# Performance work log

Measured on AMD Instinct MI355X. Metric: run time of the kernel, lower is better.

## Reference

```python
import jax, jax.numpy as jnp
import numpy as np

B, C, H, W = 8, 256, 32, 32
E = 256       # embedding_dim
K = 8192      # n_embed
COMMIT = 1.0


def setup_inputs() -> dict:
    key = jax.random.key(0)
    k1, k2, k3, k4 = jax.random.split(key, 4)
    z = jax.random.normal(k1, (B, C, H, W), dtype=jnp.float32)
    proj_w = jax.random.normal(k2, (E, C), dtype=jnp.float32) * (1.0 / np.sqrt(C))
    proj_b = jax.random.normal(k3, (E,), dtype=jnp.float32) * 0.01
    # torch init: uniform(-1/n_embed, 1/n_embed)
    embed = jax.random.uniform(k4, (K, E), dtype=jnp.float32, minval=-1.0 / K, maxval=1.0 / K)
    return {"z": z, "proj_w": proj_w, "proj_b": proj_b, "embed": embed}


def reference(z, proj_w, proj_b, embed):
    # 1x1 conv == per-pixel linear; output in NHWC layout (matches permute(0,2,3,1))
    z_e = jnp.einsum('bchw,ec->bhwe', z, proj_w) + proj_b            # [B,H,W,E]
    flat = z_e.reshape(-1, E)                                        # [BHW,E]
    # squared euclidean distance to each codebook entry
    dist = (jnp.sum(flat * flat, axis=1, keepdims=True)
            - 2.0 * flat @ embed.T
            + jnp.sum(embed * embed, axis=1)[None, :])               # [BHW,K]
    embed_ind = jnp.argmin(dist, axis=1).reshape(B, H, W)            # int indices
    z_q = embed[embed_ind]                                           # gather -> [B,H,W,E]
    sg = jax.lax.stop_gradient
    diff = (COMMIT * jnp.mean((sg(z_q) - z_e) ** 2)
            + jnp.mean((z_q - sg(z_e)) ** 2))
    z_q_st = z_e + sg(z_q - z_e)  # straight-through estimator
    return (z_q_st, diff, embed_ind)
```

## Files before the change

### kernel.cpp

```cpp
#include <hip/hip_runtime.h>

#define OUT_ZQ   0
#define OUT_DIFF 2097152
#define OUT_IND  2097153

#define WS_AMIN   0
#define WS_A      65536
#define WS_N      98304
#define WS_EMAX   131072
#define WS_DLIST  131136
#define WS_DCNT   196672
#define WS_PART   196688
#define WS_CCNT   200784
#define WS_CND    200848
#define WS_BQ     594064
#define WS_B3V    1118352
#define WS_ZH3    1310720
#define WS_ZL3    5505024
#define WS_EH3    9699328
#define WS_EL3    13893632
#define WS_BIG_END 18087936ULL
#define CAND_CAP  98304

typedef unsigned long long u64t;
typedef __attribute__((ext_vector_type(8))) short bf16x8;
typedef __attribute__((ext_vector_type(4))) float f32x4;

__device__ inline unsigned short bf16rn(float f) {
    unsigned u = __float_as_uint(f);
    return (unsigned short)((u + 0x7fffu + ((u >> 16) & 1u)) >> 16);
}
__device__ inline float bf16tof(unsigned short h) { return __uint_as_float(((unsigned)h) << 16); }
__device__ inline float valf(u64t k) { return __uint_as_float((unsigned)(k >> 32)); }

#define INITKEY ((((u64t)0x7F7FFFFFu) << 32) | 0xFFFFu)

__global__ __launch_bounds__(256) void k_init(u64t* __restrict__ amin,
                                              int* __restrict__ dcnt,
                                              unsigned* __restrict__ e2) {
    const int i = blockIdx.x * 256 + threadIdx.x;
    amin[i] = ~0ULL;
    if (i < 4) dcnt[i] = 0;
    if (i == 4) *e2 = 0u;
}

__global__ __launch_bounds__(256) void k_ze_np(const float* __restrict__ z,
                                               const float* __restrict__ pw,
                                               const float* __restrict__ pb,
                                               float* __restrict__ ze) {
    __shared__ float lz[32][16];
    const int t   = threadIdx.x;
    const int b   = blockIdx.x >> 6;
    const int hw0 = (blockIdx.x & 63) * 16;

    float acc[16];
#pragma unroll
    for (int p = 0; p < 16; ++p) acc[p] = 0.0f;

    for (int cc = 0; cc < 256; cc += 32) {
        float4 wv[8];
        const float4* wsrc = reinterpret_cast<const float4*>(pw + (size_t)t * 256 + cc);
#pragma unroll
        for (int i = 0; i < 8; ++i) wv[i] = wsrc[i];
        float zv[2];
#pragma unroll
        for (int i = 0; i < 2; ++i) {
            const int f = t + i * 256;
            zv[i] = z[(size_t)(b * 256 + cc + (f >> 4)) * 1024 + hw0 + (f & 15)];
        }
        __syncthreads();
#pragma unroll
        for (int i = 0; i < 2; ++i) {
            const int f = t + i * 256;
            lz[f >> 4][f & 15] = zv[i];
        }
        __syncthreads();
#define ZSTEP(CL, WL) {                                                     \
    const float4 q0 = *reinterpret_cast<const float4*>(&lz[CL][0]);         \
    const float4 q1 = *reinterpret_cast<const float4*>(&lz[CL][4]);         \
    const float4 q2 = *reinterpret_cast<const float4*>(&lz[CL][8]);         \
    const float4 q3 = *reinterpret_cast<const float4*>(&lz[CL][12]);        \
    acc[0]  = __fadd_rn(acc[0],  __fmul_rn(q0.x, WL));                      \
    acc[1]  = __fadd_rn(acc[1],  __fmul_rn(q0.y, WL));                      \
    acc[2]  = __fadd_rn(acc[2],  __fmul_rn(q0.z, WL));                      \
    acc[3]  = __fadd_rn(acc[3],  __fmul_rn(q0.w, WL));                      \
    acc[4]  = __fadd_rn(acc[4],  __fmul_rn(q1.x, WL));                      \
    acc[5]  = __fadd_rn(acc[5],  __fmul_rn(q1.y, WL));                      \
    acc[6]  = __fadd_rn(acc[6],  __fmul_rn(q1.z, WL));                      \
    acc[7]  = __fadd_rn(acc[7],  __fmul_rn(q1.w, WL));                      \
    acc[8]  = __fadd_rn(acc[8],  __fmul_rn(q2.x, WL));                      \
    acc[9]  = __fadd_rn(acc[9],  __fmul_rn(q2.y, WL));                      \
    acc[10] = __fadd_rn(acc[10], __fmul_rn(q2.z, WL));                      \
    acc[11] = __fadd_rn(acc[11], __fmul_rn(q2.w, WL));                      \
    acc[12] = __fadd_rn(acc[12], __fmul_rn(q3.x, WL));                      \
    acc[13] = __fadd_rn(acc[13], __fmul_rn(q3.y, WL));                      \
    acc[14] = __fadd_rn(acc[14], __fmul_rn(q3.z, WL));                      \
    acc[15] = __fadd_rn(acc[15], __fmul_rn(q3.w, WL)); }
#pragma unroll
        for (int c8 = 0; c8 < 8; ++c8) {
            const float4 wq = wv[c8];
            ZSTEP(c8 * 4 + 0, wq.x)
            ZSTEP(c8 * 4 + 1, wq.y)
            ZSTEP(c8 * 4 + 2, wq.z)
            ZSTEP(c8 * 4 + 3, wq.w)
        }
#undef ZSTEP
    }
    const float bb = pb[t];
#pragma unroll
    for (int p = 0; p < 16; ++p)
        ze[(size_t)(b * 1024 + hw0 + p) * 256 + t] = __fadd_rn(acc[p], bb);
}

__global__ __launch_bounds__(256) void k_rowstats(const float* __restrict__ ze,
                                                  const float* __restrict__ embed,
                                                  float* __restrict__ A,
                                                  float* __restrict__ Nf,
                                                  unsigned* __restrict__ e2) {
    const int gid = blockIdx.x * 256 + threadIdx.x;
    const float* row = (gid < 8192) ? (ze + (size_t)gid * 256)
                                    : (embed + (size_t)(gid - 8192) * 256);
    float blk[2];
#pragma unroll
    for (int half = 0; half < 2; ++half) {
        const float4* r4 = reinterpret_cast<const float4*>(row + half * 128);
        float r[8];
#pragma unroll
        for (int i = 0; i < 16; ++i) {
            const float4 a = r4[i * 2], b = r4[i * 2 + 1];
            const float s[8] = {__fmul_rn(a.x, a.x), __fmul_rn(a.y, a.y),
                                __fmul_rn(a.z, a.z), __fmul_rn(a.w, a.w),
                                __fmul_rn(b.x, b.x), __fmul_rn(b.y, b.y),
                                __fmul_rn(b.z, b.z), __fmul_rn(b.w, b.w)};
            if (i == 0) {
#pragma unroll
                for (int j = 0; j < 8; ++j) r[j] = s[j];
            } else {
#pragma unroll
                for (int j = 0; j < 8; ++j) r[j] = __fadd_rn(r[j], s[j]);
            }
        }
        blk[half] = __fadd_rn(__fadd_rn(__fadd_rn(r[0], r[1]), __fadd_rn(r[2], r[3])),
                              __fadd_rn(__fadd_rn(r[4], r[5]), __fadd_rn(r[6], r[7])));
    }
    const float res = __fadd_rn(blk[0], blk[1]);
    if (gid < 8192) A[gid] = res;
    else {
        Nf[gid - 8192] = res;
        float mx = res;
        for (int off = 32; off; off >>= 1) mx = fmaxf(mx, __shfl_down(mx, off, 64));
        if ((threadIdx.x & 63) == 0) atomicMax(e2, __float_as_uint(mx));
    }
}

__global__ __launch_bounds__(256) void k_cvt(const float* __restrict__ ze,
                                             const float* __restrict__ embed,
                                             unsigned short* __restrict__ zh3,
                                             unsigned short* __restrict__ zl3,
                                             unsigned short* __restrict__ eh3,
                                             unsigned short* __restrict__ el3,
                                             int* __restrict__ ccnt) {
    const int gid = blockIdx.x * 256 + threadIdx.x;
    if (gid == 0) *ccnt = 0;
    const int row = gid >> 5;
    const int c0  = (gid & 31) * 8;
    const bool isz = (row < 8192);
    const float* src = (isz ? ze + (size_t)row * 256 : embed + (size_t)(row - 8192) * 256) + c0;
    const float4 v0 = reinterpret_cast<const float4*>(src)[0];
    const float4 v1 = reinterpret_cast<const float4*>(src)[1];
    float x[8] = {v0.x, v0.y, v0.z, v0.w, v1.x, v1.y, v1.z, v1.w};
    if (isz) {
#pragma unroll
        for (int i = 0; i < 8; ++i) x[i] = __fmul_rn(2.0f, x[i]);
    }
    unsigned short hv[8], lv[8];
#pragma unroll
    for (int i = 0; i < 8; ++i) {
        hv[i] = bf16rn(x[i]);
        lv[i] = bf16rn(__fsub_rn(x[i], bf16tof(hv[i])));
    }
    const int ci = c0 >> 5, lg = (c0 >> 3) & 3;
    if (isz) {
        const int pt = row >> 6, ti = (row >> 4) & 3, lr = row & 15;
        const int lane = lg * 16 + lr;
        const size_t off = ((size_t)(ci * 128 + pt) * 4 + ti) * 512 + (size_t)lane * 8;
        *reinterpret_cast<ushort4*>(zh3 + off)     = make_ushort4(hv[0], hv[1], hv[2], hv[3]);
        *reinterpret_cast<ushort4*>(zh3 + off + 4) = make_ushort4(hv[4], hv[5], hv[6], hv[7]);
        *reinterpret_cast<ushort4*>(zl3 + off)     = make_ushort4(lv[0], lv[1], lv[2], lv[3]);
        *reinterpret_cast<ushort4*>(zl3 + off + 4) = make_ushort4(lv[4], lv[5], lv[6], lv[7]);
    } else {
        const int k = row - 8192;
        const int ks = k >> 11, ksub = (k >> 8) & 7, w = (k >> 6) & 3, tj = (k >> 4) & 3, lr = k & 15;
        const int lane = lg * 16 + lr;
        const size_t off = (((size_t)((ks * 8 + ksub) * 8 + ci) * 16) + w * 4 + tj) * 512 + (size_t)lane * 8;
        *reinterpret_cast<ushort4*>(eh3 + off)     = make_ushort4(hv[0], hv[1], hv[2], hv[3]);
        *reinterpret_cast<ushort4*>(eh3 + off + 4) = make_ushort4(hv[4], hv[5], hv[6], hv[7]);
        *reinterpret_cast<ushort4*>(el3 + off)     = make_ushort4(lv[0], lv[1], lv[2], lv[3]);
        *reinterpret_cast<ushort4*>(el3 + off + 4) = make_ushort4(lv[4], lv[5], lv[6], lv[7]);
    }
}

__global__ __launch_bounds__(256, 2) void k_mfma(const float* __restrict__ A,
                                                 const float* __restrict__ Nf,
                                                 const unsigned short* __restrict__ zh3,
                                                 const unsigned short* __restrict__ zl3,
                                                 const unsigned short* __restrict__ eh3,
                                                 const unsigned short* __restrict__ el3,
                                                 u64t* __restrict__ bq12,
                                                 float* __restrict__ b3v) {
    __shared__ u64t  mrgk[64][4][2];
    __shared__ float mrgv[64][4];
    const int t = threadIdx.x;
    const int ks = blockIdx.x & 3, pt = blockIdx.x >> 2;
    const int pix0 = pt * 64;
    const int w = t >> 6, l = t & 63;
    const int lg = l >> 4, lr = l & 15;

    float a_reg[4][4];
#pragma unroll
    for (int ti = 0; ti < 4; ++ti)
#pragma unroll
        for (int r = 0; r < 4; ++r)
            a_reg[ti][r] = A[pix0 + ti * 16 + lg * 4 + r];

    u64t b1[4][4], b2[4][4];
    float bv[4][4];
#pragma unroll
    for (int ti = 0; ti < 4; ++ti)
#pragma unroll
        for (int r = 0; r < 4; ++r) { b1[ti][r] = INITKEY; b2[ti][r] = INITKEY; bv[ti][r] = 3.402823466e+38f; }

    const size_t zoff0 = (size_t)pt * 2048 + (size_t)l * 8;
    for (int ksub = 0; ksub < 8; ++ksub) {
        f32x4 acc[4][4];
#pragma unroll
        for (int ti = 0; ti < 4; ++ti)
#pragma unroll
            for (int tj = 0; tj < 4; ++tj) acc[ti][tj] = (f32x4)(0.0f);

        const size_t ebase = (size_t)(ks * 8 + ksub) * 65536 + (size_t)w * 2048 + (size_t)l * 8;
#pragma unroll 2
        for (int ci = 0; ci < 8; ++ci) {
            const size_t zo = zoff0 + (size_t)ci * 262144;
            const size_t eo = ebase + (size_t)ci * 8192;
            bf16x8 az[4], alz[4], be[4], ble[4];
#pragma unroll
            for (int ti = 0; ti < 4; ++ti) {
                az[ti]  = *reinterpret_cast<const bf16x8*>(zh3 + zo + (size_t)ti * 512);
                alz[ti] = *reinterpret_cast<const bf16x8*>(zl3 + zo + (size_t)ti * 512);
            }
#pragma unroll
            for (int tj = 0; tj < 4; ++tj) {
                be[tj]  = *reinterpret_cast<const bf16x8*>(eh3 + eo + (size_t)tj * 512);
                ble[tj] = *reinterpret_cast<const bf16x8*>(el3 + eo + (size_t)tj * 512);
            }
#pragma unroll
            for (int tj = 0; tj < 4; ++tj)
#pragma unroll
                for (int ti = 0; ti < 4; ++ti) {
                    acc[ti][tj] = __builtin_amdgcn_mfma_f32_16x16x32_bf16(az[ti],  be[tj],  acc[ti][tj], 0, 0, 0);
                    acc[ti][tj] = __builtin_amdgcn_mfma_f32_16x16x32_bf16(az[ti],  ble[tj], acc[ti][tj], 0, 0, 0);
                    acc[ti][tj] = __builtin_amdgcn_mfma_f32_16x16x32_bf16(alz[ti], be[tj],  acc[ti][tj], 0, 0, 0);
                }
        }
#pragma unroll
        for (int tj = 0; tj < 4; ++tj) {
            const int kk = ks * 2048 + ksub * 256 + w * 64 + tj * 16 + lr;
            const float nk = Nf[kk];
#pragma unroll
            for (int ti = 0; ti < 4; ++ti)
#pragma unroll
                for (int r = 0; r < 4; ++r) {
                    const float vv = __fadd_rn(__fsub_rn(a_reg[ti][r], acc[ti][tj][r]), nk);
                    const u64t key = ((u64t)__float_as_uint(vv) << 32) | (unsigned)kk;
                    if (key < b2[ti][r]) {
                        bv[ti][r] = valf(b2[ti][r]);
                        if (key < b1[ti][r]) { b2[ti][r] = b1[ti][r]; b1[ti][r] = key; }
                        else                 { b2[ti][r] = key; }
                    } else {
                        bv[ti][r] = fminf(bv[ti][r], vv);
                    }
                }
        }
    }
#pragma unroll
    for (int ti = 0; ti < 4; ++ti)
#pragma unroll
        for (int r = 0; r < 4; ++r) {
            u64t k1 = b1[ti][r], k2 = b2[ti][r];
            float v3 = bv[ti][r];
#pragma unroll
            for (int m = 1; m <= 8; m <<= 1) {
                const u64t o1 = __shfl_xor(k1, m, 64);
                const u64t o2 = __shfl_xor(k2, m, 64);
                const float ov = __shfl_xor(v3, m, 64);
                const u64t n1 = (k1 < o1) ? k1 : o1;
                const u64t X  = (k1 < o1) ? o1 : k1;
                const u64t Y  = (k2 < o2) ? k2 : o2;
                const u64t n2 = (X < Y) ? X : Y;
                const u64t t4 = (X < Y) ? Y : X;
                v3 = fminf(fminf(v3, ov), valf(t4));
                k1 = n1; k2 = n2;
            }
            b1[ti][r] = k1; b2[ti][r] = k2; bv[ti][r] = v3;
        }
    if (lr == 0) {
#pragma unroll
        for (int ti = 0; ti < 4; ++ti)
#pragma unroll
            for (int r = 0; r < 4; ++r) {
                const int pxl = ti * 16 + lg * 4 + r;
                mrgk[pxl][w][0] = b1[ti][r];
                mrgk[pxl][w][1] = b2[ti][r];
                mrgv[pxl][w]    = bv[ti][r];
            }
    }
    __syncthreads();
    if (t < 64) {
        u64t K1 = INITKEY, K2 = INITKEY;
        float V3 = 3.402823466e+38f;
#pragma unroll
        for (int w4 = 0; w4 < 4; ++w4) {
            const u64t o1 = mrgk[t][w4][0], o2 = mrgk[t][w4][1];
            const float ov = mrgv[t][w4];
            const u64t n1 = (K1 < o1) ? K1 : o1;
            const u64t X  = (K1 < o1) ? o1 : K1;
            const u64t Y  = (K2 < o2) ? K2 : o2;
            const u64t n2 = (X < Y) ? X : Y;
            const u64t t4 = (X < Y) ? Y : X;
            V3 = fminf(fminf(V3, ov), valf(t4));
            K1 = n1; K2 = n2;
        }
        bq12[((size_t)(ks * 2 + 0)) * 8192 + pix0 + t] = K1;
        bq12[((size_t)(ks * 2 + 1)) * 8192 + pix0 + t] = K2;
        b3v[(size_t)ks * 8192 + pix0 + t] = V3;
    }
}

__global__ __launch_bounds__(256) void k_sel(const float* __restrict__ A,
                                             const u64t* __restrict__ bq12,
                                             const float* __restrict__ b3v,
                                             unsigned short* __restrict__ dlist,
                                             int* __restrict__ dcnt,
                                             int* __restrict__ ccnt,
                                             unsigned* __restrict__ cnd) {
    const int px = blockIdx.x * 256 + threadIdx.x;
    const int lane = threadIdx.x & 63;
    u64t k1[4], k2[4];
    float v3[4];
#pragma unroll
    for (int s = 0; s < 4; ++s) {
        k1[s] = bq12[((size_t)(s * 2 + 0)) * 8192 + px];
        k2[s] = bq12[((size_t)(s * 2 + 1)) * 8192 + px];
        v3[s] = b3v[(size_t)s * 8192 + px];
    }
    float m = valf(k1[0]);
#pragma unroll
    for (int s = 1; s < 4; ++s) m = fminf(m, valf(k1[s]));
    const float a = A[px];
    const unsigned eb = (__float_as_uint(a + 0.125f) >> 23) & 255u;
    const float up = __uint_as_float((eb - 23u) << 23);
    const float thresh = m + 4.5f * up + 1.0e-5f;

    unsigned cand[8];
    int nc = 0;
#pragma unroll
    for (int s = 0; s < 4; ++s) {
        if (valf(k1[s]) <= thresh) cand[nc++] = ((unsigned)px << 16) | (unsigned)(k1[s] & 0xffffu);
        if (valf(k2[s]) <= thresh) cand[nc++] = ((unsigned)px << 16) | (unsigned)(k2[s] & 0xffffu);
        if (v3[s] <= thresh) {
            const int pos = atomicAdd(&dcnt[s], 1);
            if (pos < 8192) dlist[s * 8192 + pos] = (unsigned short)px;
        }
    }
    int sc = nc;
#pragma unroll
    for (int o = 1; o < 64; o <<= 1) {
        const int n = __shfl_up(sc, o, 64);
        if (lane >= o) sc += n;
    }
    int base = 0;
    if (lane == 63) base = atomicAdd(ccnt, sc);
    base = __shfl(base, 63, 64);
    const int off = base + sc - nc;
    for (int j = 0; j < nc; ++j)
        if (off + j < CAND_CAP) cnd[off + j] = cand[j];
}

__global__ __launch_bounds__(256) void k_cand(const float* __restrict__ ze,
                                              const float* __restrict__ embed,
                                              const float* __restrict__ A,
                                              const float* __restrict__ Nf,
                                              const int* __restrict__ ccnt,
                                              const unsigned* __restrict__ cnd,
                                              u64t* __restrict__ amin) {
    int cnt = *ccnt; if (cnt > CAND_CAP) cnt = CAND_CAP;
    for (int i = blockIdx.x * 256 + threadIdx.x; i < cnt; i += 32768) {
        const unsigned pk = cnd[i];
        const int px = pk >> 16, k = pk & 0xffffu;
        const float4* zr = reinterpret_cast<const float4*>(ze + (size_t)px * 256);
        const float4* er = reinterpret_cast<const float4*>(embed + (size_t)k * 256);
        float acc = 0.0f;
        for (int c4 = 0; c4 < 64; ++c4) {
            const float4 z4 = zr[c4], e4 = er[c4];
            acc = fmaf(__fmul_rn(2.0f, z4.x), e4.x, acc);
            acc = fmaf(__fmul_rn(2.0f, z4.y), e4.y, acc);
            acc = fmaf(__fmul_rn(2.0f, z4.z), e4.z, acc);
            acc = fmaf(__fmul_rn(2.0f, z4.w), e4.w, acc);
        }
        const float v = __fadd_rn(__fsub_rn(A[px], acc), Nf[k]);
        atomicMin(&amin[px], ((u64t)__float_as_uint(v) << 32) | (unsigned)k);
    }
}

__global__ __launch_bounds__(256) void k_deep(const float* __restrict__ ze,
                                              const float* __restrict__ embed,
                                              const float* __restrict__ A,
                                              const float* __restrict__ Nf,
                                              const unsigned short* __restrict__ dlist,
                                              const int* __restrict__ dcnt,
                                              u64t* __restrict__ amin) {
    __shared__ float lz2[256];
    __shared__ float sa[1];
    __shared__ u64t lw4[4];
    const int t = threadIdx.x;
    int n0 = dcnt[0], n1 = dcnt[1], n2 = dcnt[2], n3 = dcnt[3];
    n0 = (n0 > 8192) ? 8192 : n0;  n1 = (n1 > 8192) ? 8192 : n1;
    n2 = (n2 > 8192) ? 8192 : n2;  n3 = (n3 > 8192) ? 8192 : n3;
    const int tot = (n0 + n1 + n2 + n3) * 8;

    for (int it = blockIdx.x; it < tot; it += gridDim.x) {
        const int q = it >> 3, slice = it & 7;
        int s, pxi;
        if (q < n0)                { s = 0; pxi = q; }
        else if (q < n0 + n1)      { s = 1; pxi = q - n0; }
        else if (q < n0 + n1 + n2) { s = 2; pxi = q - n0 - n1; }
        else                       { s = 3; pxi = q - n0 - n1 - n2; }
        const int px = dlist[s * 8192 + pxi];

        __syncthreads();
        lz2[t] = __fmul_rn(2.0f, ze[(size_t)px * 256 + t]);
        if (t == 0) sa[0] = A[px];
        __syncthreads();

        const int k = s * 2048 + slice * 256 + t;
        const float4* er = reinterpret_cast<const float4*>(embed + (size_t)k * 256);
        float acc = 0.0f;
#pragma unroll 8
        for (int c4 = 0; c4 < 64; ++c4) {
            const float4 e4 = er[c4];
            acc = fmaf(lz2[c4 * 4 + 0], e4.x, acc);
            acc = fmaf(lz2[c4 * 4 + 1], e4.y, acc);
            acc = fmaf(lz2[c4 * 4 + 2], e4.z, acc);
            acc = fmaf(lz2[c4 * 4 + 3], e4.w, acc);
        }
        const float v = __fadd_rn(__fsub_rn(sa[0], acc), Nf[k]);
        u64t key = ((u64t)__float_as_uint(v) << 32) | (unsigned)k;
#pragma unroll
        for (int m = 1; m <= 32; m <<= 1) {
            const u64t o = __shfl_xor(key, m, 64);
            key = (o < key) ? o : key;
        }
        if ((t & 63) == 0) lw4[t >> 6] = key;
        __syncthreads();
        if (t == 0) {
            u64t bk = lw4[0];
            bk = (lw4[1] < bk) ? lw4[1] : bk;
            bk = (lw4[2] < bk) ? lw4[2] : bk;
            bk = (lw4[3] < bk) ? lw4[3] : bk;
            atomicMin(&amin[px], bk);
        }
    }
}

__global__ __launch_bounds__(256, 2) void k_dist_r10(const float* __restrict__ ze,
                                                     const float* __restrict__ embed,
                                                     const float* __restrict__ A,
                                                     const float* __restrict__ Nf,
                                                     u64t* __restrict__ amin) {
    __shared__ __align__(16) char smem[49152];
    float (*le)[128] = reinterpret_cast<float (*)[128]>(smem);
    float (*z2)[256] = reinterpret_cast<float (*)[256]>(smem + 16384);
    u64t* red = reinterpret_cast<u64t*>(smem);

    const int t    = threadIdx.x;
    const int ks   = blockIdx.x & 31;
    const int pt   = blockIdx.x >> 5;
    const int pix0 = pt * 256;
    const int k0   = ks * 256;
    const int tp   = t & 15, tk = t >> 4;
    const int er   = t >> 1, eh2 = (t & 1) * 16;

    float best[16];
    int   bidx[16];
#pragma unroll
    for (int i = 0; i < 16; ++i) { best[i] = 3.402823466e+38f; bidx[i] = 0x7fffffff; }

    float Ai[16];
#pragma unroll
    for (int q = 0; q < 4; ++q)
#pragma unroll
        for (int m = 0; m < 4; ++m)
            Ai[q * 4 + m] = A[pix0 + (q * 16 + tp) * 4 + m];

    for (int kc = 0; kc < 256; kc += 128) {
        float acc[16][8];
#pragma unroll
        for (int i = 0; i < 16; ++i)
#pragma unroll
            for (int j = 0; j < 8; ++j) acc[i][j] = 0.0f;
        const int kbase = k0 + kc + tk * 8;
        for (int cc = 0; cc < 256; cc += 32) {
            float4 se[4], sz[8];
            const float4* esrc = reinterpret_cast<const float4*>(
                embed + (size_t)(k0 + kc + er) * 256 + cc + eh2);
#pragma unroll
            for (int m = 0; m < 4; ++m) se[m] = esrc[m];
            const float4* zsrc = reinterpret_cast<const float4*>(
                ze + (size_t)(pix0 + t) * 256 + cc);
#pragma unroll
            for (int m = 0; m < 8; ++m) sz[m] = zsrc[m];
            __syncthreads();
#pragma unroll
            for (int m = 0; m < 4; ++m) {
                le[eh2 + m * 4 + 0][er] = se[m].x;
                le[eh2 + m * 4 + 1][er] = se[m].y;
                le[eh2 + m * 4 + 2][er] = se[m].z;
                le[eh2 + m * 4 + 3][er] = se[m].w;
            }
#pragma unroll
            for (int m = 0; m < 8; ++m) {
                z2[m * 4 + 0][t] = __fmul_rn(2.0f, sz[m].x);
                z2[m * 4 + 1][t] = __fmul_rn(2.0f, sz[m].y);
                z2[m * 4 + 2][t] = __fmul_rn(2.0f, sz[m].z);
                z2[m * 4 + 3][t] = __fmul_rn(2.0f, sz[m].w);
            }
            __syncthreads();
#pragma unroll 2
            for (int c = 0; c < 32; ++c) {
                const float4 e0 = *reinterpret_cast<const float4*>(&le[c][tk * 8]);
                const float4 e1 = *reinterpret_cast<const float4*>(&le[c][tk * 8 + 4]);
                float4 zq[4];
#pragma unroll
                for (int q = 0; q < 4; ++q)
                    zq[q] = *reinterpret_cast<const float4*>(&z2[c][(q * 16 + tp) * 4]);
#define FMA8(i, zv)                                          \
    acc[i][0] = fmaf(zv, e0.x, acc[i][0]);                   \
    acc[i][1] = fmaf(zv, e0.y, acc[i][1]);                   \
    acc[i][2] = fmaf(zv, e0.z, acc[i][2]);                   \
    acc[i][3] = fmaf(zv, e0.w, acc[i][3]);                   \
    acc[i][4] = fmaf(zv, e1.x, acc[i][4]);                   \
    acc[i][5] = fmaf(zv, e1.y, acc[i][5]);                   \
    acc[i][6] = fmaf(zv, e1.z, acc[i][6]);                   \
    acc[i][7] = fmaf(zv, e1.w, acc[i][7]);
#pragma unroll
                for (int q = 0; q < 4; ++q) {
                    FMA8(q * 4 + 0, zq[q].x)
                    FMA8(q * 4 + 1, zq[q].y)
                    FMA8(q * 4 + 2, zq[q].z)
                    FMA8(q * 4 + 3, zq[q].w)
                }
#undef FMA8
            }
        }
        const float4 n0 = *reinterpret_cast<const float4*>(&Nf[kbase]);
        const float4 n1 = *reinterpret_cast<const float4*>(&Nf[kbase + 4]);
        const float nk[8] = {n0.x, n0.y, n0.z, n0.w, n1.x, n1.y, n1.z, n1.w};
#pragma unroll
        for (int j = 0; j < 8; ++j) {
            const int k = kbase + j;
#pragma unroll
            for (int i = 0; i < 16; ++i) {
                const float v = __fadd_rn(__fsub_rn(Ai[i], acc[i][j]), nk[j]);
                if (v < best[i]) { best[i] = v; bidx[i] = k; }
            }
        }
    }
    __syncthreads();
#pragma unroll
    for (int i = 0; i < 16; ++i) {
        const int px = ((i >> 2) * 16 + tp) * 4 + (i & 3);
        const unsigned u = __float_as_uint(best[i]);
        red[px * 17 + tk] = ((u64t)u << 32) | (unsigned)bidx[i];
    }
    __syncthreads();
    {
        u64t bvv = ~0ULL;
#pragma unroll 4
        for (int q2 = 0; q2 < 16; ++q2) {
            const u64t v = red[t * 17 + q2];
            bvv = (v < bvv) ? v : bvv;
        }
        atomicMin(&amin[pix0 + t], bvv);
    }
}

__global__ __launch_bounds__(256) void k_combine(const u64t* __restrict__ amin,
                                                 float* __restrict__ out_ind) {
    const int nn = blockIdx.x * 256 + threadIdx.x;
    out_ind[nn] = (float)(unsigned)(amin[nn] & 0xffffffffULL);
}

__global__ __launch_bounds__(256) void k_gather(const float* __restrict__ embed,
                                                float* __restrict__ out,
                                                const float* __restrict__ out_ind,
                                                float* __restrict__ part) {
    __shared__ double wsum[4];
    const int t = threadIdx.x;
    const int g = t >> 5, ll = t & 31;
    const int nn = blockIdx.x * 8 + g;
    const int idx = (int)(out_ind[nn] + 0.5f);
    const float4* ev4 = reinterpret_cast<const float4*>(embed + (size_t)idx * 256);
    float4* zp = reinterpret_cast<float4*>(out + (size_t)nn * 256);
    double sm = 0.0;
#pragma unroll
    for (int r = 0; r < 2; ++r) {
        const float4 ev = ev4[ll + r * 32];
        const float4 zv = zp[ll + r * 32];
        const double dx = (double)ev.x - zv.x, dy = (double)ev.y - zv.y;
        const double dz = (double)ev.z - zv.z, dw = (double)ev.w - zv.w;
        sm += dx * dx + dy * dy + dz * dz + dw * dw;
        zp[ll + r * 32] = ev;
    }
    for (int off = 32; off; off >>= 1) sm += __shfl_down(sm, off, 64);
    const int wid = t >> 6, lane = t & 63;
    if (lane == 0) wsum[wid] = sm;
    __syncthreads();
    if (t == 0) part[blockIdx.x] = (float)(wsum[0] + wsum[1] + wsum[2] + wsum[3]);
}

__global__ __launch_bounds__(256) void k_final(const float* __restrict__ part,
                                               float* __restrict__ out_diff) {
    __shared__ double wsum[4];
    double sm = 0.0;
#pragma unroll
    for (int i = 0; i < 4; ++i) sm += (double)part[threadIdx.x + i * 256];
    for (int off = 32; off; off >>= 1) sm += __shfl_down(sm, off, 64);
    const int wid = threadIdx.x >> 6, lane = threadIdx.x & 63;
    if (lane == 0) wsum[wid] = sm;
    __syncthreads();
    if (threadIdx.x == 0)
        out_diff[0] = (float)(2.0 * (wsum[0] + wsum[1] + wsum[2] + wsum[3]) / 2097152.0);
}

extern "C" void kernel_launch(void* const* d_in, const int* in_sizes, int n_in,
                              void* d_out, int out_size, void* d_ws, size_t ws_size,
                              hipStream_t stream) {
    const float* z     = (const float*)d_in[0];
    const float* pw    = (const float*)d_in[1];
    const float* pb    = (const float*)d_in[2];
    const float* embed = (const float*)d_in[3];
    float* out = (float*)d_out;
    char*  ws  = (char*)d_ws;

    u64t*           amin  = (u64t*)(ws + WS_AMIN);
    float*          A     = (float*)(ws + WS_A);
    float*          Nf    = (float*)(ws + WS_N);
    unsigned*       e2    = (unsigned*)(ws + WS_EMAX);
    unsigned short* dlist = (unsigned short*)(ws + WS_DLIST);
    int*            dcnt  = (int*)(ws + WS_DCNT);
    float*          part  = (float*)(ws + WS_PART);

    float* ze       = out + OUT_ZQ;
    float* out_diff = out + OUT_DIFF;
    float* out_ind  = out + OUT_IND;

    const bool big = (ws_size >= WS_BIG_END);

    k_init    <<<32,   256, 0, stream>>>(amin, dcnt, e2);
    k_ze_np   <<<512,  256, 0, stream>>>(z, pw, pb, ze);
    k_rowstats<<<64,   256, 0, stream>>>(ze, embed, A, Nf, e2);
    if (big) {
        int*            ccnt = (int*)(ws + WS_CCNT);
        unsigned*       cnd  = (unsigned*)(ws + WS_CND);
        u64t*           bq12 = (u64t*)(ws + WS_BQ);
        float*          b3v  = (float*)(ws + WS_B3V);
        unsigned short* zh3  = (unsigned short*)(ws + WS_ZH3);
        unsigned short* zl3  = (unsigned short*)(ws + WS_ZL3);
        unsigned short* eh3  = (unsigned short*)(ws + WS_EH3);
        unsigned short* el3  = (unsigned short*)(ws + WS_EL3);
        k_cvt  <<<2048, 256, 0, stream>>>(ze, embed, zh3, zl3, eh3, el3, ccnt);
        k_mfma <<<512,  256, 0, stream>>>(A, Nf, zh3, zl3, eh3, el3, bq12, b3v);
        k_sel  <<<32,   256, 0, stream>>>(A, bq12, b3v, dlist, dcnt, ccnt, cnd);
        k_cand <<<128,  256, 0, stream>>>(ze, embed, A, Nf, ccnt, cnd, amin);
        k_deep <<<2048, 256, 0, stream>>>(ze, embed, A, Nf, dlist, dcnt, amin);
    } else {
        k_dist_r10<<<1024, 256, 0, stream>>>(ze, embed, A, Nf, amin);
    }
    k_combine <<<32,   256, 0, stream>>>(amin, out_ind);
    k_gather  <<<1024, 256, 0, stream>>>(embed, out + OUT_ZQ, out_ind, part);
    k_final   <<<1,    256, 0, stream>>>(part, out_diff);
}
```

Before: 232.0 us.

## Split codebook into eight slices and merge candidate selection with rescoring

The MFMA screening kernel now splits the codebook into 8 slices of 1024 instead of 4 of 2048, which doubles the grid to 1024 blocks. It stores top-2 values and indices in separate arrays. Candidate selection and exact fp32 rescoring are fused into one per-pixel kernel that writes amin directly, removing the k_init, k_sel and k_cand launches and their atomic compaction. k_deep now has each block scan a fixed range of (pixel, slice) items against a stored threshold instead of reading a compacted list. The cost is more per-thread serial dot products in k_selres, possible load imbalance, and more deep-fallback items to scan.

Result: slower. 324.9 us (+40.0%).

```diff
diff --git a/kernel.cpp b/kernel.cpp
--- a/kernel.cpp
+++ b/kernel.cpp
@@ -7,20 +7,18 @@
 #define WS_AMIN   0
 #define WS_A      65536
 #define WS_N      98304
-#define WS_EMAX   131072
-#define WS_DLIST  131136
-#define WS_DCNT   196672
-#define WS_PART   196688
-#define WS_CCNT   200784
-#define WS_CND    200848
-#define WS_BQ     594064
-#define WS_B3V    1118352
-#define WS_ZH3    1310720
-#define WS_ZL3    5505024
-#define WS_EH3    9699328
-#define WS_EL3    13893632
-#define WS_BIG_END 18087936ULL
-#define CAND_CAP  98304
+#define WS_THR    131072
+#define WS_PART   163840
+#define WS_BV1    167936
+#define WS_BI1    430080
+#define WS_BV2    561152
+#define WS_BI2    823296
+#define WS_B3V    954368
+#define WS_ZH3    1216512
+#define WS_ZL3    5410816
+#define WS_EH3    9605120
+#define WS_EL3    13799424
+#define WS_BIG_END 17993728ULL
 
 typedef unsigned long long u64t;
 typedef __attribute__((ext_vector_type(8))) short bf16x8;
@@ -34,15 +32,6 @@
 __device__ inline float valf(u64t k) { return __uint_as_float((unsigned)(k >> 32)); }
 
 #define INITKEY ((((u64t)0x7F7FFFFFu) << 32) | 0xFFFFu)
-
-__global__ __launch_bounds__(256) void k_init(u64t* __restrict__ amin,
-                                              int* __restrict__ dcnt,
-                                              unsigned* __restrict__ e2) {
-    const int i = blockIdx.x * 256 + threadIdx.x;
-    amin[i] = ~0ULL;
-    if (i < 4) dcnt[i] = 0;
-    if (i == 4) *e2 = 0u;
-}
 
 __global__ __launch_bounds__(256) void k_ze_np(const float* __restrict__ z,
                                                const float* __restrict__ pw,
@@ -115,8 +104,7 @@
 __global__ __launch_bounds__(256) void k_rowstats(const float* __restrict__ ze,
                                                   const float* __restrict__ embed,
                                                   float* __restrict__ A,
-                                                  float* __restrict__ Nf,
-                                                  unsigned* __restrict__ e2) {
+                                                  float* __restrict__ Nf) {
     const int gid = blockIdx.x * 256 + threadIdx.x;
     const float* row = (gid < 8192) ? (ze + (size_t)gid * 256)
                                     : (embed + (size_t)(gid - 8192) * 256);
@@ -145,12 +133,7 @@
     }
     const float res = __fadd_rn(blk[0], blk[1]);
     if (gid < 8192) A[gid] = res;
-    else {
-        Nf[gid - 8192] = res;
-        float mx = res;
-        for (int off = 32; off; off >>= 1) mx = fmaxf(mx, __shfl_down(mx, off, 64));
-        if ((threadIdx.x & 63) == 0) atomicMax(e2, __float_as_uint(mx));
-    }
+    else            Nf[gid - 8192] = res;
 }
 
 __global__ __launch_bounds__(256) void k_cvt(const float* __restrict__ ze,
@@ -158,10 +141,8 @@
                                              unsigned short* __restrict__ zh3,
                                              unsigned short* __restrict__ zl3,
                                              unsigned short* __restrict__ eh3,
-                                             unsigned short* __restrict__ el3,
-                                             int* __restrict__ ccnt) {
+                                             unsigned short* __restrict__ el3) {
     const int gid = blockIdx.x * 256 + threadIdx.x;
-    if (gid == 0) *ccnt = 0;
     const int row = gid >> 5;
     const int c0  = (gid & 31) * 8;
     const bool isz = (row < 8192);
@@ -190,9 +171,9 @@
         *reinterpret_cast<ushort4*>(zl3 + off + 4) = make_ushort4(lv[4], lv[5], lv[6], lv[7]);
     } else {
         const int k = row - 8192;
-        const int ks = k >> 11, ksub = (k >> 8) & 7, w = (k >> 6) & 3, tj = (k >> 4) & 3, lr = k & 15;
+        const int kblk = k >> 8, w = (k >> 6) & 3, tj = (k >> 4) & 3, lr = k & 15;
         const int lane = lg * 16 + lr;
-        const size_t off = (((size_t)((ks * 8 + ksub) * 8 + ci) * 16) + w * 4 + tj) * 512 + (size_t)lane * 8;
+        const size_t off = (((size_t)(kblk * 8 + ci) * 16) + w * 4 + tj) * 512 + (size_t)lane * 8;
         *reinterpret_cast<ushort4*>(eh3 + off)     = make_ushort4(hv[0], hv[1], hv[2], hv[3]);
         *reinterpret_cast<ushort4*>(eh3 + off + 4) = make_ushort4(hv[4], hv[5], hv[6], hv[7]);
         *reinterpret_cast<ushort4*>(el3 + off)     = make_ushort4(lv[0], lv[1], lv[2], lv[3]);
@@ -206,12 +187,15 @@
                                                  const unsigned short* __restrict__ zl3,
                                                  const unsigned short* __restrict__ eh3,
                                                  const unsigned short* __restrict__ el3,
-                                                 u64t* __restrict__ bq12,
+                                                 float* __restrict__ bv1,
+                                                 unsigned short* __restrict__ bi1,
+                                                 float* __restrict__ bv2,
+                                                 unsigned short* __restrict__ bi2,
                                                  float* __restrict__ b3v) {
     __shared__ u64t  mrgk[64][4][2];
     __shared__ float mrgv[64][4];
     const int t = threadIdx.x;
-    const int ks = blockIdx.x & 3, pt = blockIdx.x >> 2;
+    const int ks = blockIdx.x & 7, pt = blockIdx.x >> 3;
     const int pix0 = pt * 64;
     const int w = t >> 6, l = t & 63;
     const int lg = l >> 4, lr = l & 15;
@@ -231,14 +215,14 @@
         for (int r = 0; r < 4; ++r) { b1[ti][r] = INITKEY; b2[ti][r] = INITKEY; bv[ti][r] = 3.402823466e+38f; }
 
     const size_t zoff0 = (size_t)pt * 2048 + (size_t)l * 8;
-    for (int ksub = 0; ksub < 8; ++ksub) {
+    for (int ksub = 0; ksub < 4; ++ksub) {
         f32x4 acc[4][4];
 #pragma unroll
         for (int ti = 0; ti < 4; ++ti)
 #pragma unroll
             for (int tj = 0; tj < 4; ++tj) acc[ti][tj] = (f32x4)(0.0f);
 
-        const size_t ebase = (size_t)(ks * 8 + ksub) * 65536 + (size_t)w * 2048 + (size_t)l * 8;
+        const size_t ebase = (size_t)(ks * 4 + ksub) * 65536 + (size_t)w * 2048 + (size_t)l * 8;
 #pragma unroll 2
         for (int ci = 0; ci < 8; ++ci) {
             const size_t zo = zoff0 + (size_t)ci * 262144;
@@ -265,7 +249,7 @@
         }
 #pragma unroll
         for (int tj = 0; tj < 4; ++tj) {
-            const int kk = ks * 2048 + ksub * 256 + w * 64 + tj * 16 + lr;
+            const int kk = ks * 1024 + ksub * 256 + w * 64 + tj * 16 + lr;
             const float nk = Nf[kk];
 #pragma unroll
             for (int ti = 0; ti < 4; ++ti)
@@ -331,119 +315,104 @@
             V3 = fminf(fminf(V3, ov), valf(t4));
             K1 = n1; K2 = n2;
         }
-        bq12[((size_t)(ks * 2 + 0)) * 8192 + pix0 + t] = K1;
-        bq12[((size_t)(ks * 2 + 1)) * 8192 + pix0 + t] = K2;
-        b3v[(size_t)ks * 8192 + pix0 + t] = V3;
-    }
-}
-
-__global__ __launch_bounds__(256) void k_sel(const float* __restrict__ A,
-                                             const u64t* __restrict__ bq12,
-                                             const float* __restrict__ b3v,
-                                             unsigned short* __restrict__ dlist,
-                                             int* __restrict__ dcnt,
-                                             int* __restrict__ ccnt,
-                                             unsigned* __restrict__ cnd) {
+        const size_t o = (size_t)ks * 8192 + pix0 + t;
+        bv1[o] = valf(K1);
+        bi1[o] = (unsigned short)(K1 & 0xffffu);
+        bv2[o] = valf(K2);
+        bi2[o] = (unsigned short)(K2 & 0xffffu);
+        b3v[o] = V3;
+    }
+}
+
+__device__ inline u64t np_score(const float* __restrict__ ze,
+                                const float* __restrict__ embed,
+                                const float a, const float* __restrict__ Nf,
+                                const int px, const int k) {
+    const float4* zr = reinterpret_cast<const float4*>(ze + (size_t)px * 256);
+    const float4* er = reinterpret_cast<const float4*>(embed + (size_t)k * 256);
+    float acc = 0.0f;
+    for (int c4 = 0; c4 < 64; ++c4) {
+        const float4 z4 = zr[c4], e4 = er[c4];
+        acc = fmaf(__fmul_rn(2.0f, z4.x), e4.x, acc);
+        acc = fmaf(__fmul_rn(2.0f, z4.y), e4.y, acc);
+        acc = fmaf(__fmul_rn(2.0f, z4.z), e4.z, acc);
+        acc = fmaf(__fmul_rn(2.0f, z4.w), e4.w, acc);
+    }
+    const float v = __fadd_rn(__fsub_rn(a, acc), Nf[k]);
+    return ((u64t)__float_as_uint(v) << 32) | (unsigned)k;
+}
+
+__global__ __launch_bounds__(256) void k_selres(const float* __restrict__ ze,
+                                                const float* __restrict__ embed,
+                                                const float* __restrict__ A,
+                                                const float* __restrict__ Nf,
+                                                const float* __restrict__ bv1,
+                                                const unsigned short* __restrict__ bi1,
+                                                const float* __restrict__ bv2,
+                                                const unsigned short* __restrict__ bi2,
+                                                float* __restrict__ thr,
+                                                u64t* __restrict__ amin) {
     const int px = blockIdx.x * 256 + threadIdx.x;
-    const int lane = threadIdx.x & 63;
-    u64t k1[4], k2[4];
-    float v3[4];
-#pragma unroll
-    for (int s = 0; s < 4; ++s) {
-        k1[s] = bq12[((size_t)(s * 2 + 0)) * 8192 + px];
-        k2[s] = bq12[((size_t)(s * 2 + 1)) * 8192 + px];
-        v3[s] = b3v[(size_t)s * 8192 + px];
-    }
-    float m = valf(k1[0]);
-#pragma unroll
-    for (int s = 1; s < 4; ++s) m = fminf(m, valf(k1[s]));
+    float m = bv1[px];
+#pragma unroll
+    for (int s = 1; s < 8; ++s) m = fminf(m, bv1[(size_t)s * 8192 + px]);
     const float a = A[px];
     const unsigned eb = (__float_as_uint(a + 0.125f) >> 23) & 255u;
     const float up = __uint_as_float((eb - 23u) << 23);
     const float thresh = m + 4.5f * up + 1.0e-5f;
-
-    unsigned cand[8];
-    int nc = 0;
-#pragma unroll
-    for (int s = 0; s < 4; ++s) {
-        if (valf(k1[s]) <= thresh) cand[nc++] = ((unsigned)px << 16) | (unsigned)(k1[s] & 0xffffu);
-        if (valf(k2[s]) <= thresh) cand[nc++] = ((unsigned)px << 16) | (unsigned)(k2[s] & 0xffffu);
-        if (v3[s] <= thresh) {
-            const int pos = atomicAdd(&dcnt[s], 1);
-            if (pos < 8192) dlist[s * 8192 + pos] = (unsigned short)px;
-        }
-    }
-    int sc = nc;
-#pragma unroll
-    for (int o = 1; o < 64; o <<= 1) {
-        const int n = __shfl_up(sc, o, 64);
-        if (lane >= o) sc += n;
-    }
-    int base = 0;
-    if (lane == 63) base = atomicAdd(ccnt, sc);
-    base = __shfl(base, 63, 64);
-    const int off = base + sc - nc;
-    for (int j = 0; j < nc; ++j)
-        if (off + j < CAND_CAP) cnd[off + j] = cand[j];
-}
-
-__global__ __launch_bounds__(256) void k_cand(const float* __restrict__ ze,
-                                              const float* __restrict__ embed,
-                                              const float* __restrict__ A,
-                                              const float* __restrict__ Nf,
-                                              const int* __restrict__ ccnt,
-                                              const unsigned* __restrict__ cnd,
-                                              u64t* __restrict__ amin) {
-    int cnt = *ccnt; if (cnt > CAND_CAP) cnt = CAND_CAP;
-    for (int i = blockIdx.x * 256 + threadIdx.x; i < cnt; i += 32768) {
-        const unsigned pk = cnd[i];
-        const int px = pk >> 16, k = pk & 0xffffu;
-        const float4* zr = reinterpret_cast<const float4*>(ze + (size_t)px * 256);
-        const float4* er = reinterpret_cast<const float4*>(embed + (size_t)k * 256);
-        float acc = 0.0f;
-        for (int c4 = 0; c4 < 64; ++c4) {
-            const float4 z4 = zr[c4], e4 = er[c4];
-            acc = fmaf(__fmul_rn(2.0f, z4.x), e4.x, acc);
-            acc = fmaf(__fmul_rn(2.0f, z4.y), e4.y, acc);
-            acc = fmaf(__fmul_rn(2.0f, z4.z), e4.z, acc);
-            acc = fmaf(__fmul_rn(2.0f, z4.w), e4.w, acc);
-        }
-        const float v = __fadd_rn(__fsub_rn(A[px], acc), Nf[k]);
-        atomicMin(&amin[px], ((u64t)__float_as_uint(v) << 32) | (unsigned)k);
-    }
+    thr[px] = thresh;
+
+    u64t best = ~0ULL;
+#pragma unroll
+    for (int s = 0; s < 8; ++s) {
+        const size_t o = (size_t)s * 8192 + px;
+        if (bv1[o] <= thresh) {
+            const u64t key = np_score(ze, embed, a, Nf, px, (int)(bi1[o] & 8191u));
+            best = (key < best) ? key : best;
+        }
+        if (bv2[o] <= thresh) {
+            const u64t key = np_score(ze, embed, a, Nf, px, (int)(bi2[o] & 8191u));
+            best = (key < best) ? key : best;
+        }
+    }
+    amin[px] = best;
 }
 
 __global__ __launch_bounds__(256) void k_deep(const float* __restrict__ ze,
                                               const float* __restrict__ embed,
                                               const float* __restrict__ A,
                                               const float* __restrict__ Nf,
-                                              const unsigned short* __restrict__ dlist,
-                                              const int* __restrict__ dcnt,
+                                              const float* __restrict__ thr,
+                                              const float* __restrict__ b3v,
                                               u64t* __restrict__ amin) {
     __shared__ float lz2[256];
     __shared__ float sa[1];
     __shared__ u64t lw4[4];
+    __shared__ int list[128];
+    __shared__ int nact;
     const int t = threadIdx.x;
-    int n0 = dcnt[0], n1 = dcnt[1], n2 = dcnt[2], n3 = dcnt[3];
-    n0 = (n0 > 8192) ? 8192 : n0;  n1 = (n1 > 8192) ? 8192 : n1;
-    n2 = (n2 > 8192) ? 8192 : n2;  n3 = (n3 > 8192) ? 8192 : n3;
-    const int tot = (n0 + n1 + n2 + n3) * 8;
-
-    for (int it = blockIdx.x; it < tot; it += gridDim.x) {
-        const int q = it >> 3, slice = it & 7;
-        int s, pxi;
-        if (q < n0)                { s = 0; pxi = q; }
-        else if (q < n0 + n1)      { s = 1; pxi = q - n0; }
-        else if (q < n0 + n1 + n2) { s = 2; pxi = q - n0 - n1; }
-        else                       { s = 3; pxi = q - n0 - n1 - n2; }
-        const int px = dlist[s * 8192 + pxi];
-
+    const int base = blockIdx.x * 128;
+
+    if (t == 0) nact = 0;
+    __syncthreads();
+    if (t < 128) {
+        const int it = base + t;
+        const int px = it >> 5, s = (it >> 2) & 7;
+        if (b3v[(size_t)s * 8192 + px] <= thr[px]) {
+            const int p = atomicAdd(&nact, 1);
+            list[p] = it;
+        }
+    }
+    __syncthreads();
+    const int n = nact;
+    for (int i = 0; i < n; ++i) {
+        const int it = list[i];
+        const int px = it >> 5, s = (it >> 2) & 7, slice = it & 3;
         __syncthreads();
         lz2[t] = __fmul_rn(2.0f, ze[(size_t)px * 256 + t]);
         if (t == 0) sa[0] = A[px];
         __syncthreads();
-
-        const int k = s * 2048 + slice * 256 + t;
+        const int k = s * 1024 + slice * 256 + t;
         const float4* er = reinterpret_cast<const float4*>(embed + (size_t)k * 256);
         float acc = 0.0f;
 #pragma unroll 8
@@ -471,6 +440,10 @@
             atomicMin(&amin[px], bk);
         }
     }
+}
+
+__global__ __launch_bounds__(256) void k_init(u64t* __restrict__ amin) {
+    amin[blockIdx.x * 256 + threadIdx.x] = ~0ULL;
 }
 
 __global__ __launch_bounds__(256, 2) void k_dist_r10(const float* __restrict__ ze,
@@ -653,13 +626,11 @@
     float* out = (float*)d_out;
     char*  ws  = (char*)d_ws;
 
-    u64t*           amin  = (u64t*)(ws + WS_AMIN);
-    float*          A     = (float*)(ws + WS_A);
-    float*          Nf    = (float*)(ws + WS_N);
-    unsigned*       e2    = (unsigned*)(ws + WS_EMAX);
-    unsigned short* dlist = (unsigned short*)(ws + WS_DLIST);
-    int*            dcnt  = (int*)(ws + WS_DCNT);
-    float*          part  = (float*)(ws + WS_PART);
+    u64t*  amin = (u64t*)(ws + WS_AMIN);
+    float* A    = (float*)(ws + WS_A);
+    float* Nf   = (float*)(ws + WS_N);
+    float* thr  = (float*)(ws + WS_THR);
+    float* part = (float*)(ws + WS_PART);
 
     float* ze       = out + OUT_ZQ;
     float* out_diff = out + OUT_DIFF;
@@ -667,24 +638,24 @@
 
     const bool big = (ws_size >= WS_BIG_END);
 
-    k_init    <<<32,   256, 0, stream>>>(amin, dcnt, e2);
     k_ze_np   <<<512,  256, 0, stream>>>(z, pw, pb, ze);
-    k_rowstats<<<64,   256, 0, stream>>>(ze, embed, A, Nf, e2);
+    k_rowstats<<<64,   256, 0, stream>>>(ze, embed, A, Nf);
     if (big) {
-        int*            ccnt = (int*)(ws + WS_CCNT);
-        unsigned*       cnd  = (unsigned*)(ws + WS_CND);
-        u64t*           bq12 = (u64t*)(ws + WS_BQ);
-        float*          b3v  = (float*)(ws + WS_B3V);
-        unsigned short* zh3  = (unsigned short*)(ws + WS_ZH3);
-        unsigned short* zl3  = (unsigned short*)(ws + WS_ZL3);
-        unsigned short* eh3  = (unsigned short*)(ws + WS_EH3);
-        unsigned short* el3  = (unsigned short*)(ws + WS_EL3);
-        k_cvt  <<<2048, 256, 0, stream>>>(ze, embed, zh3, zl3, eh3, el3, ccnt);
-        k_mfma <<<512,  256, 0, stream>>>(A, Nf, zh3, zl3, eh3, el3, bq12, b3v);
-        k_sel  <<<32,   256, 0, stream>>>(A, bq12, b3v, dlist, dcnt, ccnt, cnd);
-        k_cand <<<128,  256, 0, stream>>>(ze, embed, A, Nf, ccnt, cnd, amin);
-        k_deep <<<2048, 256, 0, stream>>>(ze, embed, A, Nf, dlist, dcnt, amin);
+        float*          bv1 = (float*)(ws + WS_BV1);
+        unsigned short* bi1 = (unsigned short*)(ws + WS_BI1);
+        float*          bv2 = (float*)(ws + WS_BV2);
+        unsigned short* bi2 = (unsigned short*)(ws + WS_BI2);
+        float*          b3v = (float*)(ws + WS_B3V);
+        unsigned short* zh3 = (unsigned short*)(ws + WS_ZH3);
+        unsigned short* zl3 = (unsigned short*)(ws + WS_ZL3);
+        unsigned short* eh3 = (unsigned short*)(ws + WS_EH3);
+        unsigned short* el3 = (unsigned short*)(ws + WS_EL3);
+        k_cvt   <<<2048, 256, 0, stream>>>(ze, embed, zh3, zl3, eh3, el3);
+        k_mfma  <<<1024, 256, 0, stream>>>(A, Nf, zh3, zl3, eh3, el3, bv1, bi1, bv2, bi2, b3v);
+        k_selres<<<32,   256, 0, stream>>>(ze, embed, A, Nf, bv1, bi1, bv2, bi2, thr, amin);
+        k_deep  <<<2048, 256, 0, stream>>>(ze, embed, A, Nf, thr, b3v, amin);
     } else {
+        k_init    <<<32,   256, 0, stream>>>(amin);
         k_dist_r10<<<1024, 256, 0, stream>>>(ze, embed, A, Nf, amin);
     }
     k_combine <<<32,   256, 0, stream>>>(amin, out_ind);
```
